# Kernel tuning notes

Measured on AMD Instinct MI355X. Metric: run time of the kernel, lower is better.

The kernel has to match this reference:

```python
import jax, jax.numpy as jnp
import numpy as np

N, E, D, H = 100000, 1600000, 128, 2
D2 = D * H  # conv2 output dim = out_dim * heads = 256


def setup_inputs() -> dict:
    key = jax.random.key(0)
    ks = jax.random.split(key, 9)
    x = jax.random.normal(ks[0], (N, D), dtype=jnp.float32)
    edge_index = jax.random.randint(ks[1], (2, E), 0, N, dtype=jnp.int64)
    edge_weight = jax.random.uniform(ks[2], (E,), dtype=jnp.float32)
    s = 1.0 / np.sqrt(D)
    W_rel1 = jax.random.normal(ks[3], (D, D), dtype=jnp.float32) * s
    W_root1 = jax.random.normal(ks[4], (D, D), dtype=jnp.float32) * s
    b1 = jnp.zeros((D,), dtype=jnp.float32)
    W_rel2 = jax.random.normal(ks[5], (D, D2), dtype=jnp.float32) * s
    W_root2 = jax.random.normal(ks[6], (D, D2), dtype=jnp.float32) * s
    b2 = jnp.zeros((D2,), dtype=jnp.float32)
    return {"x": x, "edge_index": edge_index, "edge_weight": edge_weight,
            "W_rel1": W_rel1, "b1": b1, "W_root1": W_root1,
            "W_rel2": W_rel2, "b2": b2, "W_root2": W_root2}


def _graph_conv(x, src, dst, edge_weight, W_rel, b, W_root, n_nodes):
    # message: w_e * x_src ; aggregate: mean over incoming edges at dst
    msgs = x[src] * edge_weight[:, None]                       # [E, D]
    summed = jax.ops.segment_sum(msgs, dst, num_segments=n_nodes)  # [N, D]
    cnt = jax.ops.segment_sum(jnp.ones((src.shape[0],), x.dtype), dst,
                              num_segments=n_nodes)
    mean = summed / jnp.maximum(cnt, 1.0)[:, None]
    # GraphConv: lin_rel(aggr) + lin_root(x); bias only on lin_rel
    return mean @ W_rel + b + x @ W_root


def reference(x, edge_index, edge_weight, W_rel1, b1, W_root1, W_rel2, b2, W_root2):
    src, dst = edge_index[0], edge_index[1]
    n = x.shape[0]
    h = _graph_conv(x, src, dst, edge_weight, W_rel1, b1, W_root1, n)
    out = _graph_conv(h, src, dst, edge_weight, W_rel2, b2, W_root2, n)
    return out
```

## Files before the change

kernel.cpp:

```cpp
#include <hip/hip_runtime.h>
#include <hip/hip_bf16.h>

#define D_IN 128
#define SORT_CHUNK 4096
#define NBUCK 256

typedef __attribute__((ext_vector_type(8))) short bf16x8;
typedef __attribute__((ext_vector_type(4))) float f32x4;


__global__ __launch_bounds__(256) void scan_block_sums(const int* __restrict__ in,
                                                       int* __restrict__ partial,
                                                       int M) {
    __shared__ int sdata[256];
    int b = blockIdx.x, t = threadIdx.x;
    int base = b * 1024 + t * 4;
    int s = 0;
#pragma unroll
    for (int i = 0; i < 4; ++i) {
        int idx = base + i;
        if (idx < M) s += in[idx];
    }
    sdata[t] = s;
    __syncthreads();
    for (int off = 128; off > 0; off >>= 1) {
        if (t < off) sdata[t] += sdata[t + off];
        __syncthreads();
    }
    if (t == 0) partial[b] = sdata[0];
}

__global__ void scan_partials(int* __restrict__ partial, int nb) {
    if (threadIdx.x == 0 && blockIdx.x == 0) {
        int run = 0;
        for (int i = 0; i < nb; ++i) {
            int t = partial[i];
            partial[i] = run;
            run += t;
        }
    }
}

__global__ __launch_bounds__(256) void scan_final(const int* __restrict__ in,
                                                  const int* __restrict__ partial,
                                                  int* __restrict__ outS,
                                                  int M) {
    __shared__ int sdata[256];
    int b = blockIdx.x, t = threadIdx.x;
    int base = b * 1024 + t * 4;
    int v[4];
    int s = 0;
#pragma unroll
    for (int i = 0; i < 4; ++i) {
        int idx = base + i;
        v[i] = (idx < M) ? in[idx] : 0;
        s += v[i];
    }
    sdata[t] = s;
    __syncthreads();
    for (int o = 1; o < 256; o <<= 1) {
        int tmp = 0;
        if (t >= o) tmp = sdata[t - o];
        __syncthreads();
        sdata[t] += tmp;
        __syncthreads();
    }
    int run = partial[b] + (sdata[t] - s);
#pragma unroll
    for (int i = 0; i < 4; ++i) {
        int idx = base + i;
        if (idx < M) outS[idx] = run;
        run += v[i];
    }
}


__global__ __launch_bounds__(256) void bucket_hist_kernel(const int* __restrict__ dst,
                                                          int* __restrict__ bh,
                                                          long long E, int N, int nbe) {
    __shared__ int cnt[NBUCK];
    cnt[threadIdx.x] = 0;
    __syncthreads();
    long long base = (long long)blockIdx.x * SORT_CHUNK;
    long long end = base + SORT_CHUNK;
    if (end > E) end = E;
    for (long long i = base + threadIdx.x; i < end; i += 256) {
        int b = (int)(((long long)dst[i] << 8) / N);
        atomicAdd(&cnt[b], 1);
    }
    __syncthreads();
    bh[threadIdx.x * nbe + blockIdx.x] = cnt[threadIdx.x];
}

__global__ __launch_bounds__(256) void bucket_scatter_kernel(const int* __restrict__ src,
                                                             const int* __restrict__ dst,
                                                             const float* __restrict__ ew,
                                                             const int* __restrict__ S,
                                                             int2* __restrict__ tmp_edges,
                                                             int* __restrict__ tmp_dst,
                                                             long long E, int N, int nbe) {
    __shared__ int base_lds[NBUCK];
    __shared__ int cnt[NBUCK];
    base_lds[threadIdx.x] = S[threadIdx.x * nbe + blockIdx.x];
    cnt[threadIdx.x] = 0;
    __syncthreads();
    long long b0 = (long long)blockIdx.x * SORT_CHUNK;
    long long e1 = b0 + SORT_CHUNK;
    if (e1 > E) e1 = E;
    for (long long i = b0 + threadIdx.x; i < e1; i += 256) {
        int d = dst[i];
        int b = (int)(((long long)d << 8) / N);
        int p = base_lds[b] + atomicAdd(&cnt[b], 1);
        tmp_edges[p] = make_int2(src[i], __float_as_int(ew[i]));
        tmp_dst[p] = d;
    }
}

__global__ __launch_bounds__(256) void bucket_sort_kernel(const int* __restrict__ S,
                                                          const int2* __restrict__ tmp_edges,
                                                          const int* __restrict__ tmp_dst,
                                                          int2* __restrict__ edges,
                                                          int* __restrict__ hist,
                                                          int* __restrict__ off,
                                                          long long E, int N, int nbe) {
    __shared__ int cnt[512];
    __shared__ int tsum[256];
    __shared__ int pos[512];
    const int b = blockIdx.x, t = threadIdx.x;
    const int lo = (int)(((long long)b * N + 255) >> 8);
    const int hi = (int)(((long long)(b + 1) * N + 255) >> 8);
    const int start = S[b * nbe];
    const int end = (b == NBUCK - 1) ? (int)E : S[(b + 1) * nbe];

    cnt[t] = 0;
    cnt[t + 256] = 0;
    __syncthreads();
    for (int i = start + t; i < end; i += 256)
        atomicAdd(&cnt[tmp_dst[i] - lo], 1);
    __syncthreads();

    int a0 = cnt[2 * t], a1 = cnt[2 * t + 1];
    tsum[t] = a0 + a1;
    __syncthreads();
    for (int o = 1; o < 256; o <<= 1) {
        int v = (t >= o) ? tsum[t - o] : 0;
        __syncthreads();
        tsum[t] += v;
        __syncthreads();
    }
    int excl = tsum[t] - (a0 + a1);
    pos[2 * t]     = start + excl;
    pos[2 * t + 1] = start + excl + a0;

    int d0 = lo + 2 * t, d1 = lo + 2 * t + 1;
    if (d0 < hi) { hist[d0] = a0; off[d0] = start + excl + a0; }
    if (d1 < hi) { hist[d1] = a1; off[d1] = start + excl + a0 + a1; }
    __syncthreads();

    for (int i = start + t; i < end; i += 256) {
        int d = tmp_dst[i] - lo;
        int r = atomicAdd(&pos[d], 1);
        edges[r] = tmp_edges[i];
    }
}


__global__ __launch_bounds__(256) void conv_x_kernel(const float* __restrict__ x,
                                                     __hip_bfloat16* __restrict__ xb,
                                                     long long total4) {
    long long i = (long long)blockIdx.x * 256 + threadIdx.x;
    if (i >= total4) return;
    float4 v = reinterpret_cast<const float4*>(x)[i];
    union { ushort4 u; __hip_bfloat162 h2[2]; } o;
    o.h2[0] = __float22bfloat162_rn(make_float2(v.x, v.y));
    o.h2[1] = __float22bfloat162_rn(make_float2(v.z, v.w));
    reinterpret_cast<ushort4*>(xb)[i] = o.u;
}

template <int DOUT>
__global__ __launch_bounds__(256) void conv_w_kernel(const float* __restrict__ Wrel,
                                                     const float* __restrict__ Wroot,
                                                     __hip_bfloat16* __restrict__ Wt) {
    int idx = blockIdx.x * 256 + threadIdx.x;
    if (idx >= DOUT * 256) return;
    int j = idx >> 8;
    int k = idx & 255;
    float v = (k < 128) ? Wrel[(size_t)k * DOUT + j] : Wroot[(size_t)(k - 128) * DOUT + j];
    Wt[idx] = __float2bfloat16(v);
}

__global__ __launch_bounds__(256) void aggregate_kernel(const __hip_bfloat16* __restrict__ featb,
                                                        const int2* __restrict__ edges,
                                                        const int* __restrict__ off,
                                                        const int* __restrict__ hist,
                                                        __hip_bfloat16* __restrict__ aggb,
                                                        int N) {
    int node = blockIdx.x * 4 + (threadIdx.x >> 6);
    if (node >= N) return;
    int lane = threadIdx.x & 63;
    int cnt = hist[node];
    int end = off[node];
    int start = end - cnt;
    float inv = 1.0f / fmaxf((float)cnt, 1.0f);

    const __hip_bfloat162* f2 = reinterpret_cast<const __hip_bfloat162*>(featb);
    float ax = 0.f, ay = 0.f;
    int e = start;
    for (; e + 7 < end; e += 8) {
        int2 ed[8];
#pragma unroll
        for (int i = 0; i < 8; ++i) ed[i] = edges[e + i];
#pragma unroll
        for (int i = 0; i < 8; ++i) {
            float w = __int_as_float(ed[i].y);
            float2 v = __bfloat1622float2(f2[(size_t)ed[i].x * 64 + lane]);
            ax += w * v.x;
            ay += w * v.y;
        }
    }
    for (; e + 3 < end; e += 4) {
        int2 ed[4];
#pragma unroll
        for (int i = 0; i < 4; ++i) ed[i] = edges[e + i];
#pragma unroll
        for (int i = 0; i < 4; ++i) {
            float w = __int_as_float(ed[i].y);
            float2 v = __bfloat1622float2(f2[(size_t)ed[i].x * 64 + lane]);
            ax += w * v.x;
            ay += w * v.y;
        }
    }
    for (; e < end; ++e) {
        int2 ed = edges[e];
        float w = __int_as_float(ed.y);
        float2 v = __bfloat1622float2(f2[(size_t)ed.x * 64 + lane]);
        ax += w * v.x;
        ay += w * v.y;
    }
    reinterpret_cast<__hip_bfloat162*>(aggb)[(size_t)node * 64 + lane] =
        __float22bfloat162_rn(make_float2(ax * inv, ay * inv));
}

template <int DOUT, bool OUT_BF16>
__global__ __launch_bounds__(256) void gemm_mfma2(const __hip_bfloat16* __restrict__ Arel,
                                                  const __hip_bfloat16* __restrict__ Aroot,
                                                  const __hip_bfloat16* __restrict__ Wt,
                                                  const float* __restrict__ bias,
                                                  void* __restrict__ outp,
                                                  int M) {
    constexpr int NY = DOUT / 128;
    const int nb = gridDim.x;
    const int orig = blockIdx.x;
    const int xcd = orig & 7;
    const int lid = orig >> 3;
    const int q = nb >> 3, r = nb & 7;
    const int wgid = (xcd < r ? xcd * (q + 1) : r * (q + 1) + (xcd - r) * q) + lid;

    const int ty = wgid % NY;
    const int tx = wgid / NY;
    const int tid = threadIdx.x;
    const int lane = tid & 63;
    const int wave = tid >> 6;
    const int lr = lane & 15;
    const int lk = lane >> 4;
    const int mbase = tx * 128 + (wave >> 1) * 64;
    const int nbase = ty * 128 + (wave & 1) * 64;

    const short* arow[4];
    const short* xrow[4];
#pragma unroll
    for (int mi = 0; mi < 4; ++mi) {
        int row = mbase + mi * 16 + lr;
        int rc = row < M ? row : M - 1;
        arow[mi] = (const short*)Arel  + (size_t)rc * 128 + lk * 8;
        xrow[mi] = (const short*)Aroot + (size_t)rc * 128 + lk * 8;
    }
    const short* wrow[4];
#pragma unroll
    for (int ni = 0; ni < 4; ++ni)
        wrow[ni] = (const short*)Wt + (size_t)(nbase + ni * 16 + lr) * 256 + lk * 8;

    f32x4 zero = {0.f, 0.f, 0.f, 0.f};
    f32x4 acc[4][4];
#pragma unroll
    for (int mi = 0; mi < 4; ++mi)
#pragma unroll
        for (int ni = 0; ni < 4; ++ni) acc[mi][ni] = zero;

#pragma unroll
    for (int kk = 0; kk < 8; ++kk) {
        bf16x8 a[4], b[4];
#pragma unroll
        for (int mi = 0; mi < 4; ++mi)
            a[mi] = (kk < 4)
                ? *reinterpret_cast<const bf16x8*>(arow[mi] + kk * 32)
                : *reinterpret_cast<const bf16x8*>(xrow[mi] + (kk - 4) * 32);
#pragma unroll
        for (int ni = 0; ni < 4; ++ni)
            b[ni] = *reinterpret_cast<const bf16x8*>(wrow[ni] + kk * 32);
#pragma unroll
        for (int mi = 0; mi < 4; ++mi)
#pragma unroll
            for (int ni = 0; ni < 4; ++ni)
                acc[mi][ni] = __builtin_amdgcn_mfma_f32_16x16x32_bf16(a[mi], b[ni], acc[mi][ni], 0, 0, 0);
    }

#pragma unroll
    for (int mi = 0; mi < 4; ++mi)
#pragma unroll
        for (int ni = 0; ni < 4; ++ni) {
            int col = nbase + ni * 16 + lr;
            float bv = bias[col];
#pragma unroll
            for (int rr = 0; rr < 4; ++rr) {
                int row = mbase + mi * 16 + lk * 4 + rr;
                if (row < M) {
                    float v = acc[mi][ni][rr] + bv;
                    if (OUT_BF16)
                        ((__hip_bfloat16*)outp)[(size_t)row * DOUT + col] = __float2bfloat16(v);
                    else
                        ((float*)outp)[(size_t)row * DOUT + col] = v;
                }
            }
        }
}


extern "C" void kernel_launch(void* const* d_in, const int* in_sizes, int n_in,
                              void* d_out, int out_size, void* d_ws, size_t ws_size,
                              hipStream_t stream) {
    const float* x      = (const float*)d_in[0];
    const int*   ei     = (const int*)d_in[1];
    const float* ew     = (const float*)d_in[2];
    const float* Wrel1  = (const float*)d_in[3];
    const float* b1     = (const float*)d_in[4];
    const float* Wroot1 = (const float*)d_in[5];
    const float* Wrel2  = (const float*)d_in[6];
    const float* b2     = (const float*)d_in[7];
    const float* Wroot2 = (const float*)d_in[8];
    float* out = (float*)d_out;

    const int N = in_sizes[0] / D_IN;
    const long long E = in_sizes[2];
    const int* src = ei;
    const int* dst = ei + E;

    const int nbe = (int)((E + SORT_CHUNK - 1) / SORT_CHUNK);
    const int M = nbe * NBUCK;
    const int nbM = (M + 1023) / 1024;

    int* hist = (int*)d_ws;
    int* off  = hist + N;
    int* part = off + N;
    int2* edges = (int2*)(part + 128);
    __hip_bfloat16* agg1b = (__hip_bfloat16*)(edges + E);
    __hip_bfloat16* xb    = agg1b + (size_t)N * D_IN;
    __hip_bfloat16* agg2b = xb    + (size_t)N * D_IN;
    __hip_bfloat16* hb    = agg2b + (size_t)N * D_IN;
    __hip_bfloat16* Wt1   = hb    + (size_t)N * D_IN;
    __hip_bfloat16* Wt2   = Wt1   + 128 * 256;

    int* bh      = (int*)agg1b;
    int* S       = bh + M;
    int* tmp_dst = S + M;
    int2* tmp_edges = (int2*)agg2b;

    bucket_hist_kernel<<<nbe, 256, 0, stream>>>(dst, bh, E, N, nbe);
    scan_block_sums<<<nbM, 256, 0, stream>>>(bh, part, M);
    scan_partials<<<1, 64, 0, stream>>>(part, nbM);
    scan_final<<<nbM, 256, 0, stream>>>(bh, part, S, M);
    bucket_scatter_kernel<<<nbe, 256, 0, stream>>>(src, dst, ew, S, tmp_edges, tmp_dst, E, N, nbe);
    bucket_sort_kernel<<<NBUCK, 256, 0, stream>>>(S, tmp_edges, tmp_dst, edges, hist, off, E, N, nbe);

    {
        long long total4 = (long long)N * D_IN / 4;
        conv_x_kernel<<<(int)((total4 + 255) / 256), 256, 0, stream>>>(x, xb, total4);
        conv_w_kernel<128><<<(128 * 256 + 255) / 256, 256, 0, stream>>>(Wrel1, Wroot1, Wt1);
        conv_w_kernel<256><<<(256 * 256 + 255) / 256, 256, 0, stream>>>(Wrel2, Wroot2, Wt2);
    }

    const int ab = (N + 3) / 4;
    const int gx = (N + 127) / 128;

    aggregate_kernel<<<ab, 256, 0, stream>>>(xb, edges, off, hist, agg1b, N);
    gemm_mfma2<128, true><<<gx * 1, 256, 0, stream>>>(agg1b, xb, Wt1, b1, hb, N);

    aggregate_kernel<<<ab, 256, 0, stream>>>(hb, edges, off, hist, agg2b, N);
    gemm_mfma2<256, false><<<gx * 2, 256, 0, stream>>>(agg2b, hb, Wt2, b2, out, N);
}
```

Before: 362.4 us.

## Fuse neighbor aggregation with MFMA GEMM per 128-row tile via LDS

Replaces the separate aggregate and GEMM kernels with one fused kernel per layer. Eight waves gather and mean-aggregate 16 nodes each into an LDS tile, then run the bf16 MFMA GEMM directly from LDS for the relational half and from global memory for the root half. This removes the global write and re-read of the aggregated bf16 buffer and two launches. In exchange, the GEMM cannot start until the slowest wave finishes gathering. The 34KB LDS tile and 512-thread blocks may lower occupancy during the latency-bound gather phase.

```diff
diff --git a/kernel.cpp b/kernel.cpp
--- a/kernel.cpp
+++ b/kernel.cpp
@@ -189,132 +189,130 @@
     Wt[idx] = __float2bfloat16(v);
 }
 
-__global__ __launch_bounds__(256) void aggregate_kernel(const __hip_bfloat16* __restrict__ featb,
-                                                        const int2* __restrict__ edges,
-                                                        const int* __restrict__ off,
-                                                        const int* __restrict__ hist,
-                                                        __hip_bfloat16* __restrict__ aggb,
-                                                        int N) {
-    int node = blockIdx.x * 4 + (threadIdx.x >> 6);
-    if (node >= N) return;
-    int lane = threadIdx.x & 63;
-    int cnt = hist[node];
-    int end = off[node];
-    int start = end - cnt;
-    float inv = 1.0f / fmaxf((float)cnt, 1.0f);
-
-    const __hip_bfloat162* f2 = reinterpret_cast<const __hip_bfloat162*>(featb);
-    float ax = 0.f, ay = 0.f;
-    int e = start;
-    for (; e + 7 < end; e += 8) {
-        int2 ed[8];
-#pragma unroll
-        for (int i = 0; i < 8; ++i) ed[i] = edges[e + i];
-#pragma unroll
-        for (int i = 0; i < 8; ++i) {
-            float w = __int_as_float(ed[i].y);
-            float2 v = __bfloat1622float2(f2[(size_t)ed[i].x * 64 + lane]);
-            ax += w * v.x;
-            ay += w * v.y;
+template <int DOUT, bool OUT_BF16>
+__global__ __launch_bounds__(512, 4) void fused_layer(const __hip_bfloat16* __restrict__ inb,
+                                                      const int2* __restrict__ edges,
+                                                      const int* __restrict__ off,
+                                                      const int* __restrict__ hist,
+                                                      const __hip_bfloat16* __restrict__ Wt,
+                                                      const float* __restrict__ bias,
+                                                      void* __restrict__ outp,
+                                                      int N) {
+    __shared__ __align__(16) short As[128 * 136];
+
+    const int tid = threadIdx.x;
+    const int w = tid >> 6;
+    const int lane = tid & 63;
+    const int rowg0 = blockIdx.x * 128;
+
+    const __hip_bfloat162* f2 = reinterpret_cast<const __hip_bfloat162*>(inb);
+    for (int i = 0; i < 16; ++i) {
+        int rloc = w * 16 + i;
+        int node = rowg0 + rloc;
+        float ax = 0.f, ay = 0.f;
+        if (node < N) {
+            int cnt = hist[node];
+            int end = off[node];
+            int start = end - cnt;
+            float inv = 1.0f / fmaxf((float)cnt, 1.0f);
+            int e = start;
+            for (; e + 7 < end; e += 8) {
+                int2 ed[8];
+#pragma unroll
+                for (int j = 0; j < 8; ++j) ed[j] = edges[e + j];
+#pragma unroll
+                for (int j = 0; j < 8; ++j) {
+                    float wgt = __int_as_float(ed[j].y);
+                    float2 v = __bfloat1622float2(f2[(size_t)ed[j].x * 64 + lane]);
+                    ax += wgt * v.x;
+                    ay += wgt * v.y;
+                }
+            }
+            for (; e < end; ++e) {
+                int2 ed = edges[e];
+                float wgt = __int_as_float(ed.y);
+                float2 v = __bfloat1622float2(f2[(size_t)ed.x * 64 + lane]);
+                ax += wgt * v.x;
+                ay += wgt * v.y;
+            }
+            ax *= inv;
+            ay *= inv;
         }
-    }
-    for (; e + 3 < end; e += 4) {
-        int2 ed[4];
-#pragma unroll
-        for (int i = 0; i < 4; ++i) ed[i] = edges[e + i];
-#pragma unroll
-        for (int i = 0; i < 4; ++i) {
-            float w = __int_as_float(ed[i].y);
-            float2 v = __bfloat1622float2(f2[(size_t)ed[i].x * 64 + lane]);
-            ax += w * v.x;
-            ay += w * v.y;
-        }
-    }
-    for (; e < end; ++e) {
-        int2 ed = edges[e];
-        float w = __int_as_float(ed.y);
-        float2 v = __bfloat1622float2(f2[(size_t)ed.x * 64 + lane]);
-        ax += w * v.x;
-        ay += w * v.y;
-    }
-    reinterpret_cast<__hip_bfloat162*>(aggb)[(size_t)node * 64 + lane] =
-        __float22bfloat162_rn(make_float2(ax * inv, ay * inv));
-}
-
-template <int DOUT, bool OUT_BF16>
-__global__ __launch_bounds__(256) void gemm_mfma2(const __hip_bfloat16* __restrict__ Arel,
-                                                  const __hip_bfloat16* __restrict__ Aroot,
-                                                  const __hip_bfloat16* __restrict__ Wt,
-                                                  const float* __restrict__ bias,
-                                                  void* __restrict__ outp,
-                                                  int M) {
-    constexpr int NY = DOUT / 128;
-    const int nb = gridDim.x;
-    const int orig = blockIdx.x;
-    const int xcd = orig & 7;
-    const int lid = orig >> 3;
-    const int q = nb >> 3, r = nb & 7;
-    const int wgid = (xcd < r ? xcd * (q + 1) : r * (q + 1) + (xcd - r) * q) + lid;
-
-    const int ty = wgid % NY;
-    const int tx = wgid / NY;
-    const int tid = threadIdx.x;
-    const int lane = tid & 63;
-    const int wave = tid >> 6;
+        *reinterpret_cast<__hip_bfloat162*>(&As[rloc * 136 + lane * 2]) =
+            __float22bfloat162_rn(make_float2(ax, ay));
+    }
+    __syncthreads();
+
+    constexpr int NI = DOUT / 64;
+    const int wr = w >> 2;
+    const int wc = w & 3;
     const int lr = lane & 15;
     const int lk = lane >> 4;
-    const int mbase = tx * 128 + (wave >> 1) * 64;
-    const int nbase = ty * 128 + (wave & 1) * 64;
-
-    const short* arow[4];
+    const int nbase = wc * (DOUT / 4);
+
+    const short* wrow[NI];
+#pragma unroll
+    for (int ni = 0; ni < NI; ++ni)
+        wrow[ni] = (const short*)Wt + (size_t)(nbase + ni * 16 + lr) * 256 + lk * 8;
+
+    int rl[4];
     const short* xrow[4];
 #pragma unroll
     for (int mi = 0; mi < 4; ++mi) {
-        int row = mbase + mi * 16 + lr;
-        int rc = row < M ? row : M - 1;
-        arow[mi] = (const short*)Arel  + (size_t)rc * 128 + lk * 8;
-        xrow[mi] = (const short*)Aroot + (size_t)rc * 128 + lk * 8;
-    }
-    const short* wrow[4];
-#pragma unroll
-    for (int ni = 0; ni < 4; ++ni)
-        wrow[ni] = (const short*)Wt + (size_t)(nbase + ni * 16 + lr) * 256 + lk * 8;
+        rl[mi] = wr * 64 + mi * 16 + lr;
+        int row = rowg0 + rl[mi];
+        int rc = row < N ? row : N - 1;
+        xrow[mi] = (const short*)inb + (size_t)rc * 128 + lk * 8;
+    }
 
     f32x4 zero = {0.f, 0.f, 0.f, 0.f};
-    f32x4 acc[4][4];
+    f32x4 acc[4][NI];
 #pragma unroll
     for (int mi = 0; mi < 4; ++mi)
 #pragma unroll
-        for (int ni = 0; ni < 4; ++ni) acc[mi][ni] = zero;
-
-#pragma unroll
-    for (int kk = 0; kk < 8; ++kk) {
-        bf16x8 a[4], b[4];
+        for (int ni = 0; ni < NI; ++ni) acc[mi][ni] = zero;
+
+#pragma unroll
+    for (int kk = 0; kk < 4; ++kk) {
+        bf16x8 a[4], b[NI];
 #pragma unroll
         for (int mi = 0; mi < 4; ++mi)
-            a[mi] = (kk < 4)
-                ? *reinterpret_cast<const bf16x8*>(arow[mi] + kk * 32)
-                : *reinterpret_cast<const bf16x8*>(xrow[mi] + (kk - 4) * 32);
-#pragma unroll
-        for (int ni = 0; ni < 4; ++ni)
+            a[mi] = *reinterpret_cast<const bf16x8*>(&As[rl[mi] * 136 + kk * 32 + lk * 8]);
+#pragma unroll
+        for (int ni = 0; ni < NI; ++ni)
             b[ni] = *reinterpret_cast<const bf16x8*>(wrow[ni] + kk * 32);
 #pragma unroll
         for (int mi = 0; mi < 4; ++mi)
 #pragma unroll
-            for (int ni = 0; ni < 4; ++ni)
+            for (int ni = 0; ni < NI; ++ni)
                 acc[mi][ni] = __builtin_amdgcn_mfma_f32_16x16x32_bf16(a[mi], b[ni], acc[mi][ni], 0, 0, 0);
     }
+#pragma unroll
+    for (int kk = 4; kk < 8; ++kk) {
+        bf16x8 a[4], b[NI];
+#pragma unroll
+        for (int mi = 0; mi < 4; ++mi)
+            a[mi] = *reinterpret_cast<const bf16x8*>(xrow[mi] + (kk - 4) * 32);
+#pragma unroll
+        for (int ni = 0; ni < NI; ++ni)
+            b[ni] = *reinterpret_cast<const bf16x8*>(wrow[ni] + kk * 32);
+#pragma unroll
+        for (int mi = 0; mi < 4; ++mi)
+#pragma unroll
+            for (int ni = 0; ni < NI; ++ni)
+                acc[mi][ni] = __builtin_amdgcn_mfma_f32_16x16x32_bf16(a[mi], b[ni], acc[mi][ni], 0, 0, 0);
+    }
 
 #pragma unroll
     for (int mi = 0; mi < 4; ++mi)
 #pragma unroll
-        for (int ni = 0; ni < 4; ++ni) {
+        for (int ni = 0; ni < NI; ++ni) {
             int col = nbase + ni * 16 + lr;
             float bv = bias[col];
 #pragma unroll
             for (int rr = 0; rr < 4; ++rr) {
-                int row = mbase + mi * 16 + lk * 4 + rr;
-                if (row < M) {
+                int row = rowg0 + wr * 64 + mi * 16 + lk * 4 + rr;
+                if (row < N) {
                     float v = acc[mi][ni][rr] + bv;
                     if (OUT_BF16)
                         ((__hip_bfloat16*)outp)[(size_t)row * DOUT + col] = __float2bfloat16(v);
@@ -353,17 +351,17 @@
     int* off  = hist + N;
     int* part = off + N;
     int2* edges = (int2*)(part + 128);
-    __hip_bfloat16* agg1b = (__hip_bfloat16*)(edges + E);
-    __hip_bfloat16* xb    = agg1b + (size_t)N * D_IN;
-    __hip_bfloat16* agg2b = xb    + (size_t)N * D_IN;
-    __hip_bfloat16* hb    = agg2b + (size_t)N * D_IN;
-    __hip_bfloat16* Wt1   = hb    + (size_t)N * D_IN;
-    __hip_bfloat16* Wt2   = Wt1   + 128 * 256;
-
-    int* bh      = (int*)agg1b;
+    __hip_bfloat16* scrA  = (__hip_bfloat16*)(edges + E);
+    __hip_bfloat16* xb    = scrA + (size_t)N * D_IN;
+    __hip_bfloat16* scrB  = xb   + (size_t)N * D_IN;
+    __hip_bfloat16* hb    = scrB + (size_t)N * D_IN;
+    __hip_bfloat16* Wt1   = hb   + (size_t)N * D_IN;
+    __hip_bfloat16* Wt2   = Wt1  + 128 * 256;
+
+    int* bh      = (int*)scrA;
     int* S       = bh + M;
     int* tmp_dst = S + M;
-    int2* tmp_edges = (int2*)agg2b;
+    int2* tmp_edges = (int2*)scrB;
 
     bucket_hist_kernel<<<nbe, 256, 0, stream>>>(dst, bh, E, N, nbe);
     scan_block_sums<<<nbM, 256, 0, stream>>>(bh, part, M);
@@ -379,12 +377,9 @@
         conv_w_kernel<256><<<(256 * 256 + 255) / 256, 256, 0, stream>>>(Wrel2, Wroot2, Wt2);
     }
 
-    const int ab = (N + 3) / 4;
     const int gx = (N + 127) / 128;
 
-    aggregate_kernel<<<ab, 256, 0, stream>>>(xb, edges, off, hist, agg1b, N);
-    gemm_mfma2<128, true><<<gx * 1, 256, 0, stream>>>(agg1b, xb, Wt1, b1, hb, N);
-
-    aggregate_kernel<<<ab, 256, 0, stream>>>(hb, edges, off, hist, agg2b, N);
-    gemm_mfma2<256, false><<<gx * 2, 256, 0, stream>>>(agg2b, hb, Wt2, b2, out, N);
-}
+    fused_layer<128, true><<<gx, 512, 0, stream>>>(xb, edges, off, hist, Wt1, b1, hb, N);
+
+    fused_layer<256, false><<<gx, 512, 0, stream>>>(hb, edges, off, hist, Wt2, b2, out, N);
+}
```

New measurement: 456.7 us. +26.0%, slower.

## Split wave into four edge groups with 16-byte row loads in aggregation

Applied to the files above, without the earlier changes.

The aggregation kernel now splits each 64-lane wave into four groups of 16 lanes. Each group handles every fourth edge and loads 8 bf16 values (16 bytes) per lane instead of 4-byte pairs. Partial sums are combined with cross-lane shuffles, and one group writes the row with a 16-byte store. This is meant to raise memory-level parallelism and cut per-edge instruction overhead in the gather. The final fp32 output store also becomes nontemporal to reduce cache pollution.

```diff
diff --git a/kernel.cpp b/kernel.cpp
--- a/kernel.cpp
+++ b/kernel.cpp
@@ -6,6 +6,7 @@
 #define NBUCK 256
 
 typedef __attribute__((ext_vector_type(8))) short bf16x8;
+typedef __attribute__((ext_vector_type(8))) unsigned short u16x8;
 typedef __attribute__((ext_vector_type(4))) float f32x4;
 
 
@@ -197,48 +198,53 @@
                                                         int N) {
     int node = blockIdx.x * 4 + (threadIdx.x >> 6);
     if (node >= N) return;
-    int lane = threadIdx.x & 63;
-    int cnt = hist[node];
-    int end = off[node];
-    int start = end - cnt;
-    float inv = 1.0f / fmaxf((float)cnt, 1.0f);
-
-    const __hip_bfloat162* f2 = reinterpret_cast<const __hip_bfloat162*>(featb);
-    float ax = 0.f, ay = 0.f;
-    int e = start;
-    for (; e + 7 < end; e += 8) {
-        int2 ed[8];
-#pragma unroll
-        for (int i = 0; i < 8; ++i) ed[i] = edges[e + i];
-#pragma unroll
-        for (int i = 0; i < 8; ++i) {
-            float w = __int_as_float(ed[i].y);
-            float2 v = __bfloat1622float2(f2[(size_t)ed[i].x * 64 + lane]);
-            ax += w * v.x;
-            ay += w * v.y;
+    const int lane = threadIdx.x & 63;
+    const int g = lane >> 4;
+    const int sub = lane & 15;
+    const int cnt = hist[node];
+    const int end = off[node];
+    const int start = end - cnt;
+    const float inv = 1.0f / fmaxf((float)cnt, 1.0f);
+
+    const ushort* fb = (const ushort*)featb;
+    float acc[8] = {0.f, 0.f, 0.f, 0.f, 0.f, 0.f, 0.f, 0.f};
+
+    int e = start + g;
+    for (; e + 4 < end; e += 8) {
+        int2 e0 = edges[e];
+        int2 e1 = edges[e + 4];
+        float w0 = __int_as_float(e0.y);
+        float w1 = __int_as_float(e1.y);
+        u16x8 r0 = *reinterpret_cast<const u16x8*>(fb + (size_t)e0.x * 128 + sub * 8);
+        u16x8 r1 = *reinterpret_cast<const u16x8*>(fb + (size_t)e1.x * 128 + sub * 8);
+#pragma unroll
+        for (int j = 0; j < 8; ++j) {
+            acc[j] += w0 * __int_as_float((unsigned)r0[j] << 16)
+                    + w1 * __int_as_float((unsigned)r1[j] << 16);
         }
     }
-    for (; e + 3 < end; e += 4) {
-        int2 ed[4];
-#pragma unroll
-        for (int i = 0; i < 4; ++i) ed[i] = edges[e + i];
-#pragma unroll
-        for (int i = 0; i < 4; ++i) {
-            float w = __int_as_float(ed[i].y);
-            float2 v = __bfloat1622float2(f2[(size_t)ed[i].x * 64 + lane]);
-            ax += w * v.x;
-            ay += w * v.y;
-        }
-    }
-    for (; e < end; ++e) {
-        int2 ed = edges[e];
-        float w = __int_as_float(ed.y);
-        float2 v = __bfloat1622float2(f2[(size_t)ed.x * 64 + lane]);
-        ax += w * v.x;
-        ay += w * v.y;
-    }
-    reinterpret_cast<__hip_bfloat162*>(aggb)[(size_t)node * 64 + lane] =
-        __float22bfloat162_rn(make_float2(ax * inv, ay * inv));
+    if (e < end) {
+        int2 e0 = edges[e];
+        float w0 = __int_as_float(e0.y);
+        u16x8 r0 = *reinterpret_cast<const u16x8*>(fb + (size_t)e0.x * 128 + sub * 8);
+#pragma unroll
+        for (int j = 0; j < 8; ++j)
+            acc[j] += w0 * __int_as_float((unsigned)r0[j] << 16);
+    }
+
+#pragma unroll
+    for (int j = 0; j < 8; ++j) {
+        acc[j] += __shfl_xor(acc[j], 16, 64);
+        acc[j] += __shfl_xor(acc[j], 32, 64);
+    }
+
+    if (g == 0) {
+        union { u16x8 u; __hip_bfloat162 h2[4]; } o;
+#pragma unroll
+        for (int j = 0; j < 4; ++j)
+            o.h2[j] = __float22bfloat162_rn(make_float2(acc[2 * j] * inv, acc[2 * j + 1] * inv));
+        *reinterpret_cast<u16x8*>((ushort*)aggb + (size_t)node * 128 + sub * 8) = o.u;
+    }
 }
 
 template <int DOUT, bool OUT_BF16>
@@ -319,7 +325,7 @@
                     if (OUT_BF16)
                         ((__hip_bfloat16*)outp)[(size_t)row * DOUT + col] = __float2bfloat16(v);
                     else
-                        ((float*)outp)[(size_t)row * DOUT + col] = v;
+                        __builtin_nontemporal_store(v, (float*)outp + (size_t)row * DOUT + col);
                 }
             }
         }
```

Result: faster. 331.6 us (-8.5%).
